# Performance work log

Hardware: AMD Instinct MI355X
Metric: run time of the kernel (lower is better)

Reference implementation:

```python
import jax, jax.numpy as jnp
import numpy as np

N = 100000
E = 1600000
NFEAT, NHID, NCLASS = 500, 128, 40


def setup_inputs() -> dict:
    key = jax.random.key(0)
    ks = jax.random.split(key, 12)
    x = jax.random.normal(ks[0], (N, NFEAT), dtype=jnp.float32)
    row = jax.random.randint(ks[1], (E,), 0, N, dtype=jnp.int32)
    col = jax.random.randint(ks[2], (E,), 0, N, dtype=jnp.int32)
    # precomputed normalized adjacency values (D^-1/2 A D^-1/2 style)
    edge_weight = jax.random.uniform(ks[3], (E,), dtype=jnp.float32) / 16.0
    def lin(k, fi, fo):
        s = 1.0 / np.sqrt(fi)
        return jax.random.uniform(k, (fi, fo), dtype=jnp.float32, minval=-s, maxval=s)
    return {
        "x": x, "row": row, "col": col, "edge_weight": edge_weight,
        "W1": lin(ks[4], NFEAT, NHID), "b1": jnp.zeros((NHID,), jnp.float32),
        "W2": lin(ks[5], NHID, NHID), "b2": jnp.zeros((NHID,), jnp.float32),
        "W3": lin(ks[6], NHID, NHID), "b3": jnp.zeros((NHID,), jnp.float32),
        "W4": lin(ks[7], NHID, NCLASS), "b4": jnp.zeros((NCLASS,), jnp.float32),
    }


def gcn_layer(h, row, col, edge_weight, W, b):
    # support = h @ W ; out = spmm(adj, support) + b  (Kipf GraphConvolution)
    support = h @ W                                   # [N, Fout]
    msgs = edge_weight[:, None] * support[col]        # [E, Fout] gather on source nodes
    agg = jax.ops.segment_sum(msgs, row, num_segments=N)  # scatter-add to dest nodes
    return agg + b


def reference(x, row, col, edge_weight, W1, b1, W2, b2, W3, b3, W4, b4):
    # dropout is identity in eval mode (training=False)
    h = jax.nn.relu(gcn_layer(x, row, col, edge_weight, W1, b1))
    h = jax.nn.relu(gcn_layer(h, row, col, edge_weight, W2, b2))
    h = jax.nn.relu(gcn_layer(h, row, col, edge_weight, W3, b3))
    h = gcn_layer(h, row, col, edge_weight, W4, b4)
    return jax.nn.log_softmax(h, axis=1)
```

## Files before the change

kernel.cpp:

```cpp
#include <hip/hip_runtime.h>
#include <cstdint>
#include <cstddef>

#define NFEAT 500
#define NHID  128
#define NCLASS 40

typedef __attribute__((ext_vector_type(8))) short bf16x8;
typedef __attribute__((ext_vector_type(4))) float f32x4;

__device__ __forceinline__ unsigned short f2bf(float f) {
    union { float f; unsigned u; } v; v.f = f;
    unsigned u = v.u;
    unsigned r = u + 0x7FFF + ((u >> 16) & 1);
    return (unsigned short)(r >> 16);
}
__device__ __forceinline__ float bf2f(unsigned short h) {
    union { unsigned u; float f; } v; v.u = ((unsigned)h) << 16; return v.f;
}


__global__ void k_hist(const int* __restrict__ row, int E, int* __restrict__ counts) {
    int i = blockIdx.x * 256 + threadIdx.x;
    if (i < E) atomicAdd(&counts[row[i]], 1);
}

__global__ void k_block_sum(const int* __restrict__ counts, int n, int* __restrict__ partials) {
    __shared__ int tmp[256];
    int i = blockIdx.x * 256 + threadIdx.x;
    tmp[threadIdx.x] = (i < n) ? counts[i] : 0;
    __syncthreads();
    for (int o = 128; o > 0; o >>= 1) {
        if (threadIdx.x < o) tmp[threadIdx.x] += tmp[threadIdx.x + o];
        __syncthreads();
    }
    if (threadIdx.x == 0) partials[blockIdx.x] = tmp[0];
}

__global__ void k_scan_partials(int* __restrict__ partials, int nb) {
    __shared__ int tmp[512];
    int t = threadIdx.x;
    int v = (t < nb) ? partials[t] : 0;
    tmp[t] = v;
    __syncthreads();
    for (int o = 1; o < 512; o <<= 1) {
        int add = (t >= o) ? tmp[t - o] : 0;
        __syncthreads();
        tmp[t] += add;
        __syncthreads();
    }
    if (t < nb) partials[t] = tmp[t] - v;
}

__global__ void k_scan_counts(int* __restrict__ counts, const int* __restrict__ partials,
                              int* __restrict__ row_ptr, int n) {
    __shared__ int tmp[256];
    int t = threadIdx.x;
    int i = blockIdx.x * 256 + t;
    int v = (i < n) ? counts[i] : 0;
    tmp[t] = v;
    __syncthreads();
    for (int o = 1; o < 256; o <<= 1) {
        int add = (t >= o) ? tmp[t - o] : 0;
        __syncthreads();
        tmp[t] += add;
        __syncthreads();
    }
    int incl = tmp[t];
    int base = partials[blockIdx.x];
    if (i < n) {
        row_ptr[i] = base + incl - v;
        counts[i] = 0;
    }
    if (i == n - 1) row_ptr[n] = base + incl;
}

__global__ void k_scatter(const int* __restrict__ row, const int* __restrict__ col,
                          const float* __restrict__ w, int E,
                          const int* __restrict__ row_ptr, int* __restrict__ cursor,
                          uint2* __restrict__ csr_cw) {
    int i = blockIdx.x * 256 + threadIdx.x;
    if (i < E) {
        int r = row[i];
        int p = row_ptr[r] + atomicAdd(&cursor[r], 1);
        csr_cw[p] = make_uint2((unsigned)col[i], __float_as_uint(w[i]));
    }
}


__global__ void k_prep_w(const float* __restrict__ W, unsigned short* __restrict__ Wt,
                         int K, int Norig, int Nt, int Kpad) {
    int idx = blockIdx.x * 256 + threadIdx.x;
    if (idx >= Nt * Kpad) return;
    int n = idx / Kpad, k = idx % Kpad;
    unsigned short v = 0;
    if (k < K && n < Norig) v = f2bf(W[(size_t)k * Norig + n]);
    Wt[idx] = v;
}


template<bool AFP32, int BN, int CN, int CPITCH>
__global__ __launch_bounds__(256) void k_gemm_mfma(const void* __restrict__ Ain,
                                                   const unsigned short* __restrict__ Wt,
                                                   unsigned short* __restrict__ C,
                                                   int M, int K, int Kpad) {
    constexpr int P  = 40;
    constexpr int NW = (BN == 128) ? 2 : 1;
    constexpr int MW = 4 / NW;
    constexpr int TM = 128 / (MW * 16);
    constexpr int TN = BN / (NW * 16);
    __shared__ unsigned short As[2][128][P];

    const int t = threadIdx.x;
    const int lane = t & 63;
    const int w = t >> 6;
    const int wm = w / NW, wn = w % NW;
    const int mbase = blockIdx.x * 128;
    const int l15 = lane & 15, quad = lane >> 4;

    const float* Af = (const float*)Ain;
    const unsigned short* Ab = (const unsigned short*)Ain;

    f32x4 acc[TM][TN];
#pragma unroll
    for (int mi = 0; mi < TM; mi++)
#pragma unroll
        for (int ni = 0; ni < TN; ni++)
            acc[mi][ni] = (f32x4){0.f, 0.f, 0.f, 0.f};

    float4 ra_f[4];
    uint4  ra_b[2];

    auto loadA = [&](int k0) {
        if (AFP32) {
#pragma unroll
            for (int p = 0; p < 4; p++) {
                int idx = p * 256 + t;
                int m = idx >> 3, ch = idx & 7;
                int gm = mbase + m, gk = k0 + ch * 4;
                float4 v = make_float4(0.f, 0.f, 0.f, 0.f);
                if (gm < M && gk + 4 <= K) v = *(const float4*)(Af + (size_t)gm * K + gk);
                ra_f[p] = v;
            }
        } else {
#pragma unroll
            for (int p = 0; p < 2; p++) {
                int idx = p * 256 + t;
                int m = idx >> 2, ch = idx & 3;
                ra_b[p] = *(const uint4*)(Ab + (size_t)(mbase + m) * Kpad + k0 + ch * 8);
            }
        }
    };
    auto storeLDS = [&](int buf) {
        if (AFP32) {
#pragma unroll
            for (int p = 0; p < 4; p++) {
                int idx = p * 256 + t;
                int m = idx >> 3, ch = idx & 7;
                float4 v = ra_f[p];
                unsigned long long pk = (unsigned long long)f2bf(v.x)
                                      | ((unsigned long long)f2bf(v.y) << 16)
                                      | ((unsigned long long)f2bf(v.z) << 32)
                                      | ((unsigned long long)f2bf(v.w) << 48);
                *(unsigned long long*)&As[buf][m][ch * 4] = pk;
            }
        } else {
#pragma unroll
            for (int p = 0; p < 2; p++) {
                int idx = p * 256 + t;
                int m = idx >> 2, ch = idx & 3;
                *(uint4*)&As[buf][m][ch * 8] = ra_b[p];
            }
        }
    };

    const int nIter = Kpad >> 5;
    loadA(0);
    storeLDS(0);
    __syncthreads();

    for (int it = 0; it < nIter; it++) {
        const int cur = it & 1;
        const int k0 = it << 5;
        const bool more = (it + 1) < nIter;
        if (more) loadA(k0 + 32);

        bf16x8 bfr[TN];
#pragma unroll
        for (int ni = 0; ni < TN; ni++)
            bfr[ni] = *(const bf16x8*)(Wt + (size_t)(wn * (TN * 16) + ni * 16 + l15) * Kpad + k0 + quad * 8);

        bf16x8 afr[TM];
#pragma unroll
        for (int mi = 0; mi < TM; mi++)
            afr[mi] = *(const bf16x8*)&As[cur][wm * (TM * 16) + mi * 16 + l15][quad * 8];

#pragma unroll
        for (int mi = 0; mi < TM; mi++)
#pragma unroll
            for (int ni = 0; ni < TN; ni++)
                acc[mi][ni] = __builtin_amdgcn_mfma_f32_16x16x32_bf16(afr[mi], bfr[ni], acc[mi][ni], 0, 0, 0);

        if (more) {
            storeLDS(cur ^ 1);
            __syncthreads();
        }
    }

#pragma unroll
    for (int mi = 0; mi < TM; mi++) {
#pragma unroll
        for (int r = 0; r < 4; r++) {
            int gm = mbase + wm * (TM * 16) + mi * 16 + quad * 4 + r;
#pragma unroll
            for (int ni = 0; ni < TN; ni++) {
                int gn = wn * (TN * 16) + ni * 16 + l15;
                if (gn < CN) C[(size_t)gm * CPITCH + gn] = f2bf(acc[mi][ni][r]);
            }
        }
    }
}


__global__ __launch_bounds__(256) void k_spmm128(const unsigned short* __restrict__ S,
                                                 const int* __restrict__ rp,
                                                 const uint2* __restrict__ cw,
                                                 const float* __restrict__ bias,
                                                 unsigned short* __restrict__ out,
                                                 int n, int do_relu) {
    int wid  = threadIdx.x >> 6;
    int lane = threadIdx.x & 63;
    int node = blockIdx.x * 4 + wid;
    if (node >= n) return;
    int s = rp[node], e = rp[node + 1];
    float a0x = 0.f, a0y = 0.f, a1x = 0.f, a1y = 0.f;
    float a2x = 0.f, a2y = 0.f, a3x = 0.f, a3y = 0.f;
    int i = s;
    for (; i + 4 <= e; i += 4) {
        uint2 e0 = cw[i], e1 = cw[i + 1], e2 = cw[i + 2], e3 = cw[i + 3];
        unsigned v0 = ((const unsigned*)(S + (size_t)e0.x * NHID))[lane];
        unsigned v1 = ((const unsigned*)(S + (size_t)e1.x * NHID))[lane];
        unsigned v2 = ((const unsigned*)(S + (size_t)e2.x * NHID))[lane];
        unsigned v3 = ((const unsigned*)(S + (size_t)e3.x * NHID))[lane];
        float w0 = __uint_as_float(e0.y), w1 = __uint_as_float(e1.y);
        float w2 = __uint_as_float(e2.y), w3 = __uint_as_float(e3.y);
        a0x = fmaf(w0, bf2f((unsigned short)v0), a0x); a0y = fmaf(w0, bf2f((unsigned short)(v0 >> 16)), a0y);
        a1x = fmaf(w1, bf2f((unsigned short)v1), a1x); a1y = fmaf(w1, bf2f((unsigned short)(v1 >> 16)), a1y);
        a2x = fmaf(w2, bf2f((unsigned short)v2), a2x); a2y = fmaf(w2, bf2f((unsigned short)(v2 >> 16)), a2y);
        a3x = fmaf(w3, bf2f((unsigned short)v3), a3x); a3y = fmaf(w3, bf2f((unsigned short)(v3 >> 16)), a3y);
    }
    for (; i < e; i++) {
        uint2 e0 = cw[i];
        unsigned v0 = ((const unsigned*)(S + (size_t)e0.x * NHID))[lane];
        float w0 = __uint_as_float(e0.y);
        a0x = fmaf(w0, bf2f((unsigned short)v0), a0x); a0y = fmaf(w0, bf2f((unsigned short)(v0 >> 16)), a0y);
    }
    float ax = (a0x + a1x) + (a2x + a3x) + bias[lane * 2];
    float ay = (a0y + a1y) + (a2y + a3y) + bias[lane * 2 + 1];
    if (do_relu) {
        ax = fmaxf(ax, 0.f);
        ay = fmaxf(ay, 0.f);
    }
    unsigned o = (unsigned)f2bf(ax) | ((unsigned)f2bf(ay) << 16);
    __builtin_nontemporal_store(o, (unsigned*)(out + (size_t)node * NHID) + lane);
}


__global__ __launch_bounds__(256) void k_spmm40_lsm(const unsigned short* __restrict__ S,
                                                    const int* __restrict__ rp,
                                                    const uint2* __restrict__ cw,
                                                    const float* __restrict__ bias,
                                                    float* __restrict__ out,
                                                    int n) {
    int wid  = threadIdx.x >> 6;
    int lane = threadIdx.x & 63;
    int node = blockIdx.x * 4 + wid;
    if (node >= n) return;
    int s = rp[node], e = rp[node + 1];
    float a0 = 0.f, a1 = 0.f, a2 = 0.f, a3 = 0.f;
    int i = s;
    bool act = lane < NCLASS;
    for (; i + 4 <= e; i += 4) {
        uint2 e0 = cw[i], e1 = cw[i + 1], e2 = cw[i + 2], e3 = cw[i + 3];
        if (act) {
            float v0 = bf2f(S[(size_t)e0.x * NCLASS + lane]);
            float v1 = bf2f(S[(size_t)e1.x * NCLASS + lane]);
            float v2 = bf2f(S[(size_t)e2.x * NCLASS + lane]);
            float v3 = bf2f(S[(size_t)e3.x * NCLASS + lane]);
            a0 = fmaf(__uint_as_float(e0.y), v0, a0);
            a1 = fmaf(__uint_as_float(e1.y), v1, a1);
            a2 = fmaf(__uint_as_float(e2.y), v2, a2);
            a3 = fmaf(__uint_as_float(e3.y), v3, a3);
        }
    }
    for (; i < e; i++) {
        uint2 e0 = cw[i];
        if (act) a0 = fmaf(__uint_as_float(e0.y), bf2f(S[(size_t)e0.x * NCLASS + lane]), a0);
    }
    float acc = (a0 + a1) + (a2 + a3);
    float logit = act ? acc + bias[lane] : -INFINITY;
    float m = logit;
#pragma unroll
    for (int o = 32; o >= 1; o >>= 1) m = fmaxf(m, __shfl_xor(m, o, 64));
    float ex = act ? expf(logit - m) : 0.f;
    float ssum = ex;
#pragma unroll
    for (int o = 32; o >= 1; o >>= 1) ssum += __shfl_xor(ssum, o, 64);
    if (act) {
        float r = logit - m - logf(ssum);
        __builtin_nontemporal_store(r, out + (size_t)node * NCLASS + lane);
    }
}


extern "C" void kernel_launch(void* const* d_in, const int* in_sizes, int n_in,
                              void* d_out, int out_size, void* d_ws, size_t ws_size,
                              hipStream_t stream) {
    const float* x  = (const float*)d_in[0];
    const int* row  = (const int*)d_in[1];
    const int* col  = (const int*)d_in[2];
    const float* ew = (const float*)d_in[3];
    const float* W1 = (const float*)d_in[4];
    const float* b1 = (const float*)d_in[5];
    const float* W2 = (const float*)d_in[6];
    const float* b2 = (const float*)d_in[7];
    const float* W3 = (const float*)d_in[8];
    const float* b3 = (const float*)d_in[9];
    const float* W4 = (const float*)d_in[10];
    const float* b4 = (const float*)d_in[11];
    float* out = (float*)d_out;

    const int Nn = in_sizes[0] / NFEAT;
    const int E  = in_sizes[1];
    const int NB = (Nn + 255) / 256;
    const int Mpad = (Nn + 127) & ~127;

    char* ws = (char*)d_ws;
    size_t off = 0;
    auto alloc = [&](size_t bytes) {
        size_t o = off;
        off = (off + bytes + 255) & ~(size_t)255;
        return o;
    };
    int*   row_ptr  = (int*)(ws + alloc((size_t)(Nn + 1) * 4));
    int*   counts   = (int*)(ws + alloc((size_t)Nn * 4));
    int*   partials = (int*)(ws + alloc((size_t)NB * 4));
    uint2* csr_cw   = (uint2*)(ws + alloc((size_t)E * 8));
    unsigned short* Sb  = (unsigned short*)(ws + alloc((size_t)Mpad * NHID * 2));
    unsigned short* Hb  = (unsigned short*)(ws + alloc((size_t)Mpad * NHID * 2));
    unsigned short* S4b = (unsigned short*)(ws + alloc((size_t)Mpad * NCLASS * 2));
    unsigned short* Wt1 = (unsigned short*)(ws + alloc((size_t)128 * 512 * 2));
    unsigned short* Wt2 = (unsigned short*)(ws + alloc((size_t)128 * 128 * 2));
    unsigned short* Wt3 = (unsigned short*)(ws + alloc((size_t)128 * 128 * 2));
    unsigned short* Wt4 = (unsigned short*)(ws + alloc((size_t)48 * 128 * 2));

    k_prep_w<<<(128 * 512 + 255) / 256, 256, 0, stream>>>(W1, Wt1, NFEAT, NHID, 128, 512);
    k_prep_w<<<(128 * 128 + 255) / 256, 256, 0, stream>>>(W2, Wt2, NHID, NHID, 128, 128);
    k_prep_w<<<(128 * 128 + 255) / 256, 256, 0, stream>>>(W3, Wt3, NHID, NHID, 128, 128);
    k_prep_w<<<(48 * 128 + 255) / 256, 256, 0, stream>>>(W4, Wt4, NHID, NCLASS, 48, 128);

    (void)hipMemsetAsync(counts, 0, (size_t)Nn * 4, stream);
    k_hist<<<(E + 255) / 256, 256, 0, stream>>>(row, E, counts);
    k_block_sum<<<NB, 256, 0, stream>>>(counts, Nn, partials);
    k_scan_partials<<<1, 512, 0, stream>>>(partials, NB);
    k_scan_counts<<<NB, 256, 0, stream>>>(counts, partials, row_ptr, Nn);
    k_scatter<<<(E + 255) / 256, 256, 0, stream>>>(row, col, ew, E, row_ptr, counts, csr_cw);

    const int gblocks = Mpad / 128;
    const int spmm_blocks = (Nn + 3) / 4;

    k_gemm_mfma<true, 128, 128, 128><<<gblocks, 256, 0, stream>>>(x, Wt1, Sb, Nn, NFEAT, 512);
    k_spmm128<<<spmm_blocks, 256, 0, stream>>>(Sb, row_ptr, csr_cw, b1, Hb, Nn, 1);
    k_gemm_mfma<false, 128, 128, 128><<<gblocks, 256, 0, stream>>>(Hb, Wt2, Sb, Nn, NHID, NHID);
    k_spmm128<<<spmm_blocks, 256, 0, stream>>>(Sb, row_ptr, csr_cw, b2, Hb, Nn, 1);
    k_gemm_mfma<false, 128, 128, 128><<<gblocks, 256, 0, stream>>>(Hb, Wt3, Sb, Nn, NHID, NHID);
    k_spmm128<<<spmm_blocks, 256, 0, stream>>>(Sb, row_ptr, csr_cw, b3, Hb, Nn, 1);
    k_gemm_mfma<false, 48, 40, 40><<<gblocks, 256, 0, stream>>>(Hb, Wt4, S4b, Nn, NHID, NHID);
    k_spmm40_lsm<<<spmm_blocks, 256, 0, stream>>>(S4b, row_ptr, csr_cw, b4, out, Nn);
}
```

Measured before the change: 859.5 us.

## Deepen GEMM prefetch pipeline, swizzle LDS A tile, raise occupancy hint

Reworks the MFMA GEMM main loop into a two-stage unrolled ping-pong. Global A tiles are prefetched two K-steps ahead into alternating register sets, and W fragments are prefetched one step ahead. The A tile in LDS is now an unpadded 32-wide layout with an XOR swizzle on 8-element chunks, in place of the padded pitch, to avoid bank conflicts. It also sets a launch-bounds occupancy hint of 3 blocks and uses a raw lgkmcnt wait plus barrier. This hides global load latency in the GEMMs, at the cost of more registers and a loop that assumes an even iteration count.

Measured after the change: 969.0 us. +12.7%, slower.

```diff
diff --git a/kernel.cpp b/kernel.cpp
--- a/kernel.cpp
+++ b/kernel.cpp
@@ -99,17 +99,18 @@
 }
 
 
+#define LDSBAR() asm volatile("s_waitcnt lgkmcnt(0)\n\ts_barrier" ::: "memory")
+
 template<bool AFP32, int BN, int CN, int CPITCH>
-__global__ __launch_bounds__(256) void k_gemm_mfma(const void* __restrict__ Ain,
-                                                   const unsigned short* __restrict__ Wt,
-                                                   unsigned short* __restrict__ C,
-                                                   int M, int K, int Kpad) {
-    constexpr int P  = 40;
+__global__ __launch_bounds__(256, 3) void k_gemm_mfma(const void* __restrict__ Ain,
+                                                      const unsigned short* __restrict__ Wt,
+                                                      unsigned short* __restrict__ C,
+                                                      int M, int K, int Kpad) {
     constexpr int NW = (BN == 128) ? 2 : 1;
     constexpr int MW = 4 / NW;
     constexpr int TM = 128 / (MW * 16);
     constexpr int TN = BN / (NW * 16);
-    __shared__ unsigned short As[2][128][P];
+    __shared__ __align__(16) unsigned short As[2][128 * 32];
 
     const int t = threadIdx.x;
     const int lane = t & 63;
@@ -128,82 +129,90 @@
         for (int ni = 0; ni < TN; ni++)
             acc[mi][ni] = (f32x4){0.f, 0.f, 0.f, 0.f};
 
-    float4 ra_f[4];
-    uint4  ra_b[2];
-
-    auto loadA = [&](int k0) {
+    const int sc = t & 3;
+    const int sm = t >> 2;
+    const int scs = sc ^ ((sm >> 1) & 3);
+
+    auto loadA_f = [&](float4* r, int k0) {
+        int gk = k0 + sc * 8;
+        const float* p0 = Af + (size_t)(mbase + sm) * K + gk;
+        const float* p1 = p0 + (size_t)64 * K;
+        bool g0 = (mbase + sm) < M;
+        bool g1 = (mbase + 64 + sm) < M;
+        bool k0ok = gk + 4 <= K, k1ok = gk + 8 <= K;
+        float4 z = make_float4(0.f, 0.f, 0.f, 0.f);
+        r[0] = (g0 && k0ok) ? *(const float4*)p0 : z;
+        r[1] = (g0 && k1ok) ? *(const float4*)(p0 + 4) : z;
+        r[2] = (g1 && k0ok) ? *(const float4*)p1 : z;
+        r[3] = (g1 && k1ok) ? *(const float4*)(p1 + 4) : z;
+    };
+    auto loadA_b = [&](uint4* r, int k0) {
+        const unsigned short* p0 = Ab + (size_t)(mbase + sm) * Kpad + k0 + sc * 8;
+        r[0] = *(const uint4*)p0;
+        r[1] = *(const uint4*)(p0 + (size_t)64 * Kpad);
+    };
+    auto pack8 = [&](float4 a, float4 b) -> uint4 {
+        uint4 u;
+        u.x = (unsigned)f2bf(a.x) | ((unsigned)f2bf(a.y) << 16);
+        u.y = (unsigned)f2bf(a.z) | ((unsigned)f2bf(a.w) << 16);
+        u.z = (unsigned)f2bf(b.x) | ((unsigned)f2bf(b.y) << 16);
+        u.w = (unsigned)f2bf(b.z) | ((unsigned)f2bf(b.w) << 16);
+        return u;
+    };
+    auto storeLDS = [&](unsigned short* buf, const float4* rf, const uint4* rb) {
+        unsigned short* d0 = buf + sm * 32 + scs * 8;
         if (AFP32) {
-#pragma unroll
-            for (int p = 0; p < 4; p++) {
-                int idx = p * 256 + t;
-                int m = idx >> 3, ch = idx & 7;
-                int gm = mbase + m, gk = k0 + ch * 4;
-                float4 v = make_float4(0.f, 0.f, 0.f, 0.f);
-                if (gm < M && gk + 4 <= K) v = *(const float4*)(Af + (size_t)gm * K + gk);
-                ra_f[p] = v;
-            }
+            *(uint4*)d0 = pack8(rf[0], rf[1]);
+            *(uint4*)(d0 + 64 * 32) = pack8(rf[2], rf[3]);
         } else {
-#pragma unroll
-            for (int p = 0; p < 2; p++) {
-                int idx = p * 256 + t;
-                int m = idx >> 2, ch = idx & 3;
-                ra_b[p] = *(const uint4*)(Ab + (size_t)(mbase + m) * Kpad + k0 + ch * 8);
-            }
-        }
-    };
-    auto storeLDS = [&](int buf) {
-        if (AFP32) {
-#pragma unroll
-            for (int p = 0; p < 4; p++) {
-                int idx = p * 256 + t;
-                int m = idx >> 3, ch = idx & 7;
-                float4 v = ra_f[p];
-                unsigned long long pk = (unsigned long long)f2bf(v.x)
-                                      | ((unsigned long long)f2bf(v.y) << 16)
-                                      | ((unsigned long long)f2bf(v.z) << 32)
-                                      | ((unsigned long long)f2bf(v.w) << 48);
-                *(unsigned long long*)&As[buf][m][ch * 4] = pk;
-            }
-        } else {
-#pragma unroll
-            for (int p = 0; p < 2; p++) {
-                int idx = p * 256 + t;
-                int m = idx >> 2, ch = idx & 3;
-                *(uint4*)&As[buf][m][ch * 8] = ra_b[p];
-            }
-        }
+            *(uint4*)d0 = rb[0];
+            *(uint4*)(d0 + 64 * 32) = rb[1];
+        }
+    };
+    auto loadB = [&](bf16x8* bf, int k0) {
+        const unsigned short* bp = Wt + (size_t)(wn * (TN * 16) + l15) * Kpad + k0 + quad * 8;
+#pragma unroll
+        for (int ni = 0; ni < TN; ni++)
+            bf[ni] = *(const bf16x8*)(bp + (size_t)(ni * 16) * Kpad);
+    };
+    auto compute = [&](const unsigned short* sbuf, const bf16x8* bf) {
+        bf16x8 afr[TM];
+        const int rcs = quad ^ ((l15 >> 1) & 3);
+#pragma unroll
+        for (int mi = 0; mi < TM; mi++) {
+            int r = wm * (TM * 16) + mi * 16 + l15;
+            afr[mi] = *(const bf16x8*)(sbuf + r * 32 + rcs * 8);
+        }
+#pragma unroll
+        for (int mi = 0; mi < TM; mi++)
+#pragma unroll
+            for (int ni = 0; ni < TN; ni++)
+                acc[mi][ni] = __builtin_amdgcn_mfma_f32_16x16x32_bf16(afr[mi], bf[ni], acc[mi][ni], 0, 0, 0);
     };
 
     const int nIter = Kpad >> 5;
-    loadA(0);
-    storeLDS(0);
-    __syncthreads();
-
-    for (int it = 0; it < nIter; it++) {
-        const int cur = it & 1;
-        const int k0 = it << 5;
-        const bool more = (it + 1) < nIter;
-        if (more) loadA(k0 + 32);
-
-        bf16x8 bfr[TN];
-#pragma unroll
-        for (int ni = 0; ni < TN; ni++)
-            bfr[ni] = *(const bf16x8*)(Wt + (size_t)(wn * (TN * 16) + ni * 16 + l15) * Kpad + k0 + quad * 8);
-
-        bf16x8 afr[TM];
-#pragma unroll
-        for (int mi = 0; mi < TM; mi++)
-            afr[mi] = *(const bf16x8*)&As[cur][wm * (TM * 16) + mi * 16 + l15][quad * 8];
-
-#pragma unroll
-        for (int mi = 0; mi < TM; mi++)
-#pragma unroll
-            for (int ni = 0; ni < TN; ni++)
-                acc[mi][ni] = __builtin_amdgcn_mfma_f32_16x16x32_bf16(afr[mi], bfr[ni], acc[mi][ni], 0, 0, 0);
-
-        if (more) {
-            storeLDS(cur ^ 1);
-            __syncthreads();
+    float4 raA_f[4], raB_f[4];
+    uint4  raA_b[2], raB_b[2];
+    bf16x8 bA[TN], bB[TN];
+
+    if (AFP32) loadA_f(raA_f, 0); else loadA_b(raA_b, 0);
+    loadB(bA, 0);
+    if (AFP32) loadA_f(raB_f, 32); else loadA_b(raB_b, 32);
+    storeLDS(As[0], raA_f, raA_b);
+    LDSBAR();
+
+    for (int it = 0; it < nIter; it += 2) {
+        if (it + 2 < nIter) { if (AFP32) loadA_f(raA_f, (it + 2) * 32); else loadA_b(raA_b, (it + 2) * 32); }
+        loadB(bB, (it + 1) * 32);
+        compute(As[0], bA);
+        storeLDS(As[1], raB_f, raB_b);
+        LDSBAR();
+        if (it + 3 < nIter) { if (AFP32) loadA_f(raB_f, (it + 3) * 32); else loadA_b(raB_b, (it + 3) * 32); }
+        if (it + 2 < nIter) loadB(bA, (it + 2) * 32);
+        compute(As[1], bB);
+        if (it + 2 < nIter) {
+            storeLDS(As[0], raA_f, raA_b);
+            LDSBAR();
         }
     }
 
```

## Replace LDS-staged GEMM with direct-to-register per-wave MFMA GEMM

Applied to the files above, without the earlier changes.

Replaces the double-buffered LDS-staged GEMM with a kernel where each wave owns 32 rows and loads A fragments straight from global memory into MFMA operands, with no shared memory or block barriers. The first layer converts fp32 x to bf16 in registers and handles the K=500 tail separately. This removes LDS traffic and __syncthreads stalls. In exchange each wave now reads the full weight tile on its own, so W is reused less within a block, and A loads are less coalesced (strided per-lane 32-byte chunks).

After: 884.4 us. 1.03x slower.

```diff
diff --git a/kernel.cpp b/kernel.cpp
--- a/kernel.cpp
+++ b/kernel.cpp
@@ -17,6 +17,15 @@
 }
 __device__ __forceinline__ float bf2f(unsigned short h) {
     union { unsigned u; float f; } v; v.u = ((unsigned)h) << 16; return v.f;
+}
+
+__device__ __forceinline__ bf16x8 cvt8(float4 a, float4 b) {
+    union { bf16x8 v; unsigned u[4]; } r;
+    r.u[0] = (unsigned)f2bf(a.x) | ((unsigned)f2bf(a.y) << 16);
+    r.u[1] = (unsigned)f2bf(a.z) | ((unsigned)f2bf(a.w) << 16);
+    r.u[2] = (unsigned)f2bf(b.x) | ((unsigned)f2bf(b.y) << 16);
+    r.u[3] = (unsigned)f2bf(b.z) | ((unsigned)f2bf(b.w) << 16);
+    return r.v;
 }
 
 
@@ -100,23 +109,17 @@
 
 
 template<bool AFP32, int BN, int CN, int CPITCH>
-__global__ __launch_bounds__(256) void k_gemm_mfma(const void* __restrict__ Ain,
-                                                   const unsigned short* __restrict__ Wt,
-                                                   unsigned short* __restrict__ C,
-                                                   int M, int K, int Kpad) {
-    constexpr int P  = 40;
-    constexpr int NW = (BN == 128) ? 2 : 1;
-    constexpr int MW = 4 / NW;
-    constexpr int TM = 128 / (MW * 16);
-    constexpr int TN = BN / (NW * 16);
-    __shared__ unsigned short As[2][128][P];
-
+__global__ __launch_bounds__(256) void k_gemm_direct(const void* __restrict__ Ain,
+                                                     const unsigned short* __restrict__ Wt,
+                                                     unsigned short* __restrict__ C,
+                                                     int M, int K, int Kpad) {
+    constexpr int TM = 2;
+    constexpr int TN = BN / 16;
     const int t = threadIdx.x;
     const int lane = t & 63;
-    const int w = t >> 6;
-    const int wm = w / NW, wn = w % NW;
-    const int mbase = blockIdx.x * 128;
     const int l15 = lane & 15, quad = lane >> 4;
+    const int wave = blockIdx.x * 4 + (t >> 6);
+    const int m0 = wave * 32;
 
     const float* Af = (const float*)Ain;
     const unsigned short* Ab = (const unsigned short*)Ain;
@@ -128,82 +131,70 @@
         for (int ni = 0; ni < TN; ni++)
             acc[mi][ni] = (f32x4){0.f, 0.f, 0.f, 0.f};
 
-    float4 ra_f[4];
-    uint4  ra_b[2];
-
-    auto loadA = [&](int k0) {
-        if (AFP32) {
-#pragma unroll
-            for (int p = 0; p < 4; p++) {
-                int idx = p * 256 + t;
-                int m = idx >> 3, ch = idx & 7;
-                int gm = mbase + m, gk = k0 + ch * 4;
-                float4 v = make_float4(0.f, 0.f, 0.f, 0.f);
-                if (gm < M && gk + 4 <= K) v = *(const float4*)(Af + (size_t)gm * K + gk);
-                ra_f[p] = v;
-            }
+    const int r0 = m0 + l15, r1 = m0 + 16 + l15;
+    bool g0 = true, g1 = true;
+    int rc0 = r0, rc1 = r1;
+    if constexpr (AFP32) {
+        g0 = r0 < M; g1 = r1 < M;
+        rc0 = g0 ? r0 : M - 1;
+        rc1 = g1 ? r1 : M - 1;
+    }
+
+    const unsigned short* bp = Wt + (size_t)l15 * Kpad + quad * 8;
+
+    const int nFull = K >> 5;
+#pragma unroll 2
+    for (int it = 0; it < nFull; it++) {
+        const int k0 = it << 5;
+        bf16x8 bfr[TN];
+#pragma unroll
+        for (int ni = 0; ni < TN; ni++)
+            bfr[ni] = *(const bf16x8*)(bp + (size_t)(ni * 16) * Kpad + k0);
+        bf16x8 afr[TM];
+        if constexpr (AFP32) {
+            const float* p0 = Af + (size_t)rc0 * K + k0 + quad * 8;
+            const float* p1 = Af + (size_t)rc1 * K + k0 + quad * 8;
+            float4 x0 = *(const float4*)p0, x1 = *(const float4*)(p0 + 4);
+            float4 y0 = *(const float4*)p1, y1 = *(const float4*)(p1 + 4);
+            float4 z = make_float4(0.f, 0.f, 0.f, 0.f);
+            if (!g0) { x0 = z; x1 = z; }
+            if (!g1) { y0 = z; y1 = z; }
+            afr[0] = cvt8(x0, x1);
+            afr[1] = cvt8(y0, y1);
         } else {
-#pragma unroll
-            for (int p = 0; p < 2; p++) {
-                int idx = p * 256 + t;
-                int m = idx >> 2, ch = idx & 3;
-                ra_b[p] = *(const uint4*)(Ab + (size_t)(mbase + m) * Kpad + k0 + ch * 8);
-            }
+            afr[0] = *(const bf16x8*)(Ab + (size_t)r0 * Kpad + k0 + quad * 8);
+            afr[1] = *(const bf16x8*)(Ab + (size_t)r1 * Kpad + k0 + quad * 8);
         }
-    };
-    auto storeLDS = [&](int buf) {
-        if (AFP32) {
-#pragma unroll
-            for (int p = 0; p < 4; p++) {
-                int idx = p * 256 + t;
-                int m = idx >> 3, ch = idx & 7;
-                float4 v = ra_f[p];
-                unsigned long long pk = (unsigned long long)f2bf(v.x)
-                                      | ((unsigned long long)f2bf(v.y) << 16)
-                                      | ((unsigned long long)f2bf(v.z) << 32)
-                                      | ((unsigned long long)f2bf(v.w) << 48);
-                *(unsigned long long*)&As[buf][m][ch * 4] = pk;
-            }
-        } else {
-#pragma unroll
-            for (int p = 0; p < 2; p++) {
-                int idx = p * 256 + t;
-                int m = idx >> 2, ch = idx & 3;
-                *(uint4*)&As[buf][m][ch * 8] = ra_b[p];
-            }
-        }
-    };
-
-    const int nIter = Kpad >> 5;
-    loadA(0);
-    storeLDS(0);
-    __syncthreads();
-
-    for (int it = 0; it < nIter; it++) {
-        const int cur = it & 1;
-        const int k0 = it << 5;
-        const bool more = (it + 1) < nIter;
-        if (more) loadA(k0 + 32);
-
-        bf16x8 bfr[TN];
-#pragma unroll
-        for (int ni = 0; ni < TN; ni++)
-            bfr[ni] = *(const bf16x8*)(Wt + (size_t)(wn * (TN * 16) + ni * 16 + l15) * Kpad + k0 + quad * 8);
-
-        bf16x8 afr[TM];
-#pragma unroll
-        for (int mi = 0; mi < TM; mi++)
-            afr[mi] = *(const bf16x8*)&As[cur][wm * (TM * 16) + mi * 16 + l15][quad * 8];
-
 #pragma unroll
         for (int mi = 0; mi < TM; mi++)
 #pragma unroll
             for (int ni = 0; ni < TN; ni++)
                 acc[mi][ni] = __builtin_amdgcn_mfma_f32_16x16x32_bf16(afr[mi], bfr[ni], acc[mi][ni], 0, 0, 0);
-
-        if (more) {
-            storeLDS(cur ^ 1);
-            __syncthreads();
+    }
+
+    if constexpr (AFP32) {
+        if (K & 31) {
+            const int k0 = nFull << 5;
+            bf16x8 bfr[TN];
+#pragma unroll
+            for (int ni = 0; ni < TN; ni++)
+                bfr[ni] = *(const bf16x8*)(bp + (size_t)(ni * 16) * Kpad + k0);
+            float va[8], vb[8];
+#pragma unroll
+            for (int j = 0; j < 8; j++) {
+                int gk = k0 + quad * 8 + j;
+                bool kk = gk < K;
+                va[j] = (g0 && kk) ? Af[(size_t)rc0 * K + gk] : 0.f;
+                vb[j] = (g1 && kk) ? Af[(size_t)rc1 * K + gk] : 0.f;
+            }
+            bf16x8 afr[TM];
+            afr[0] = cvt8(make_float4(va[0], va[1], va[2], va[3]), make_float4(va[4], va[5], va[6], va[7]));
+            afr[1] = cvt8(make_float4(vb[0], vb[1], vb[2], vb[3]), make_float4(vb[4], vb[5], vb[6], vb[7]));
+#pragma unroll
+            for (int mi = 0; mi < TM; mi++)
+#pragma unroll
+                for (int ni = 0; ni < TN; ni++)
+                    acc[mi][ni] = __builtin_amdgcn_mfma_f32_16x16x32_bf16(afr[mi], bfr[ni], acc[mi][ni], 0, 0, 0);
         }
     }
 
@@ -211,10 +202,10 @@
     for (int mi = 0; mi < TM; mi++) {
 #pragma unroll
         for (int r = 0; r < 4; r++) {
-            int gm = mbase + wm * (TM * 16) + mi * 16 + quad * 4 + r;
+            int gm = m0 + mi * 16 + quad * 4 + r;
 #pragma unroll
             for (int ni = 0; ni < TN; ni++) {
-                int gn = wn * (TN * 16) + ni * 16 + l15;
+                int gn = ni * 16 + l15;
                 if (gn < CN) C[(size_t)gm * CPITCH + gn] = f2bf(acc[mi][ni][r]);
             }
         }
@@ -369,12 +360,12 @@
     const int gblocks = Mpad / 128;
     const int spmm_blocks = (Nn + 3) / 4;
 
-    k_gemm_mfma<true, 128, 128, 128><<<gblocks, 256, 0, stream>>>(x, Wt1, Sb, Nn, NFEAT, 512);
+    k_gemm_direct<true, 128, 128, 128><<<gblocks, 256, 0, stream>>>(x, Wt1, Sb, Nn, NFEAT, 512);
     k_spmm128<<<spmm_blocks, 256, 0, stream>>>(Sb, row_ptr, csr_cw, b1, Hb, Nn, 1);
-    k_gemm_mfma<false, 128, 128, 128><<<gblocks, 256, 0, stream>>>(Hb, Wt2, Sb, Nn, NHID, NHID);
+    k_gemm_direct<false, 128, 128, 128><<<gblocks, 256, 0, stream>>>(Hb, Wt2, Sb, Nn, NHID, NHID);
     k_spmm128<<<spmm_blocks, 256, 0, stream>>>(Sb, row_ptr, csr_cw, b2, Hb, Nn, 1);
-    k_gemm_mfma<false, 128, 128, 128><<<gblocks, 256, 0, stream>>>(Hb, Wt3, Sb, Nn, NHID, NHID);
+    k_gemm_direct<false, 128, 128, 128><<<gblocks, 256, 0, stream>>>(Hb, Wt3, Sb, Nn, NHID, NHID);
     k_spmm128<<<spmm_blocks, 256, 0, stream>>>(Sb, row_ptr, csr_cw, b3, Hb, Nn, 1);
-    k_gemm_mfma<false, 48, 40, 40><<<gblocks, 256, 0, stream>>>(Hb, Wt4, S4b, Nn, NHID, NHID);
+    k_gemm_direct<false, 48, 40, 40><<<gblocks, 256, 0, stream>>>(Hb, Wt4, S4b, Nn, NHID, NHID);
     k_spmm40_lsm<<<spmm_blocks, 256, 0, stream>>>(S4b, row_ptr, csr_cw, b4, out, Nn);
 }
```
